# Performance work log

Hardware: AMD Instinct MI355X
Metric: run time of the kernel (lower is better)

## Reference

```python
import jax, jax.numpy as jnp
import numpy as np

CC_ITERS = 60  # min-label propagation + pointer doubling; covers huge diameters


def setup_inputs() -> dict:
    key = jax.random.key(0)
    k1, k2, k3, k4, k5 = jax.random.split(key, 5)
    N, C, E = 100000, 128, 800000
    x = jax.random.normal(k1, (N, C), jnp.float32)
    src = jax.random.randint(k2, (E,), 0, N)
    off = jax.random.randint(k3, (E,), 1, N)
    dst = (src + off) % N  # guarantees no self-loops (torch forward filters them)
    edge_index = jnp.stack([src, dst]).astype(jnp.int32)
    batch = jnp.zeros((N,), jnp.int32)
    W = jax.random.normal(k4, (2 * C,), jnp.float32) * 0.05
    b = (jax.random.normal(k5, (), jnp.float32) * 0.05).astype(jnp.float32)
    return {"x": x, "edge_index": edge_index, "batch": batch, "W": W, "b": b}


def _connected_components(src, dst, mask, N):
    # min-label propagation along selected edges, with path compression.
    def body(i, labels):
        ls = jnp.where(mask, labels[src], N)
        ld = jnp.where(mask, labels[dst], N)
        new = labels.at[dst].min(ls).at[src].min(ld)
        return jnp.minimum(new, new[new])  # pointer doubling
    return jax.lax.fori_loop(0, CC_ITERS, body, jnp.arange(N))


def reference(x, edge_index, batch, W, b):
    N, C = x.shape
    E = edge_index.shape[1]
    src, dst = edge_index[0], edge_index[1]

    # raw edge score: Linear(cat(x[src], x[dst])) without materializing the concat
    e = x[src] @ W[:C] + x[dst] @ W[C:] + b  # [E]
    # softmax over incoming edges of each dst node (segment softmax)
    m = jax.ops.segment_max(e, dst, num_segments=N)
    z = jnp.exp(e - m[dst])
    s = jax.ops.segment_sum(z, dst, num_segments=N)
    score = z / s[dst] + 0.5  # add_to_edge_score

    # edge selection (E > N -> quantile branch, matching torch)
    if E > N:
        q = 1.0 - (N // 2) / E
        mask = score > jnp.quantile(score, q)
    else:
        mask = score >= jnp.median(score)

    # weighted pairwise node reps for selected edges (masked instead of gathered)
    w = jnp.where(mask, score, 0.0)
    reps = (x[src] + x[dst]) * w[:, None]  # [E, C]
    mi = mask.astype(x.dtype)
    cnt = jnp.zeros((N,), x.dtype).at[src].add(mi).at[dst].add(mi)  # bincount of selected endpoints
    merged = cnt > 0
    base = jnp.where(merged[:, None], 0.0, x)  # merged nodes zeroed, untouched nodes keep x
    acc = base.at[src].add(reps).at[dst].add(reps)
    nodes = jnp.where(merged[:, None], acc / jnp.maximum(cnt, 1.0)[:, None], acc)

    # connected components over selected edges; relabel by first-occurrence order
    labels = _connected_components(src, dst, jax.lax.stop_gradient(mask), N)
    uniq = jnp.unique(labels, size=N, fill_value=N)
    cluster = jnp.searchsorted(uniq, labels)  # [N]

    new_x = jax.ops.segment_sum(nodes, cluster, num_segments=N)  # padded to N clusters

    # coalesce cluster-mapped edges: sorted unique pairs, padded with -1
    c0, c1 = cluster[src], cluster[dst]
    keys = jnp.unique(c0.astype(jnp.int64) * N + c1.astype(jnp.int64), size=E, fill_value=-1)
    valid = keys >= 0
    new_edge_index = jnp.stack([
        jnp.where(valid, keys // N, -1),
        jnp.where(valid, keys % N, -1),
    ])
    new_batch = jnp.zeros((N,), batch.dtype).at[cluster].set(batch)
    return new_x, new_edge_index, new_batch, score
```

## Files before the change

### kernel.cpp

```cpp
#include <hip/hip_runtime.h>
#include <math.h>
#include <stdint.h>

typedef unsigned long long u64;
typedef unsigned int u32;

#define NN 100000
#define CF 128
#define EE 800000

#define CAP 131072

#define EBITS 11
#define ERADIX 2048
#define STILE 2048
#define NB_E 391
#define SORT_N (NB_E * STILE)
#define MBITS 12
#define MRADIX 4096
#define NB_M 49
#define MSORT_N (NB_M * STILE)
#define HISTG_LEN 800768

#define SCTILE 2048
#define MCHUNK 16

#define ZSCALE 4503599627370496.0
#define XSCALE 32768.0f
#define XINV   (1.0f / 32768.0f)

struct Sel { u32 prefix; u32 k; };

__device__ inline u64 encD(double v) {
  u64 u = (u64)__double_as_longlong(v);
  return u ^ ((u >> 63) ? ~0ULL : 0x8000000000000000ULL);
}
__device__ inline double decD(u64 u) {
  u ^= ((u >> 63) ? 0x8000000000000000ULL : ~0ULL);
  return __longlong_as_double((long long)u);
}

__global__ void k_pq(const float* __restrict__ x, const float* __restrict__ W,
                     double* __restrict__ p, double* __restrict__ q) {
  int node = blockIdx.x * 4 + (threadIdx.x >> 6);
  int lane = threadIdx.x & 63;
  if (node >= NN) return;
  const float* xr = x + (size_t)node * CF;
  double a = (double)xr[lane] * (double)W[lane] + (double)xr[lane + 64] * (double)W[lane + 64];
  double c = (double)xr[lane] * (double)W[CF + lane] + (double)xr[lane + 64] * (double)W[CF + lane + 64];
  for (int off = 32; off; off >>= 1) { a += __shfl_xor(a, off); c += __shfl_xor(c, off); }
  if (lane == 0) { p[node] = a; q[node] = c; }
}

__global__ void k_em(const int* __restrict__ ei, const double* __restrict__ p,
                     const double* __restrict__ q, const float* __restrict__ bptr,
                     double* __restrict__ e, u64* __restrict__ menc) {
  int j = blockIdx.x * 256 + threadIdx.x;
  if (j >= EE) return;
  int s = ei[j], d = ei[EE + j];
  double ev = p[s] + q[d] + (double)bptr[0];
  e[j] = ev;
  atomicMax(&menc[d], encD(ev));
}

__global__ void k_zs(const int* __restrict__ ei, double* __restrict__ e,
                     const u64* __restrict__ menc, u64* __restrict__ sdenFx) {
  int j = blockIdx.x * 256 + threadIdx.x;
  if (j >= EE) return;
  int d = ei[EE + j];
  double z = exp(e[j] - decD(menc[d]));
  e[j] = z;
  atomicAdd(&sdenFx[d], (u64)__double2ll_rn(z * ZSCALE));
}

__global__ void k_score(const int* __restrict__ ei, const double* __restrict__ z,
                        const u64* __restrict__ sdenFx, float* __restrict__ outScore) {
  int j = blockIdx.x * 256 + threadIdx.x;
  if (j >= EE) return;
  int d = ei[EE + j];
  double s = (double)sdenFx[d] * (1.0 / ZSCALE);
  outScore[j] = (float)(z[j] / s + 0.5);
}

__global__ void k_selInit(Sel* st, u32* hist, int k0, int k1) {
  int t = blockIdx.x * 256 + threadIdx.x;
  if (t == 0) { st[0].prefix = 0x3Fu; st[0].k = (u32)k0; st[1].prefix = 0x3Fu; st[1].k = (u32)k1; }
  if (t < 512) hist[t] = 0;
}

__global__ void k_selHist(const float* __restrict__ score, const Sel* __restrict__ st,
                          u32* __restrict__ hist, int shift) {
  __shared__ u32 h[512];
  for (int i = threadIdx.x; i < 512; i += 256) h[i] = 0;
  __syncthreads();
  u32 p0 = st[0].prefix, p1 = st[1].prefix;
  for (int j = blockIdx.x * 256 + threadIdx.x; j < EE; j += gridDim.x * 256) {
    u32 u = __float_as_uint(score[j]);
    u32 d = (u >> shift) & 255u;
    if ((u >> (shift + 8)) == p0) atomicAdd(&h[d], 1u);
    if ((u >> (shift + 8)) == p1) atomicAdd(&h[256 + d], 1u);
  }
  __syncthreads();
  for (int i = threadIdx.x; i < 512; i += 256) if (h[i]) atomicAdd(&hist[i], h[i]);
}

__global__ void k_selPick(Sel* st, u32* hist) {
  if (threadIdx.x == 0) {
    for (int sel = 0; sel < 2; sel++) {
      u32 k = st[sel].k, cum = 0;
      for (int b = 0; b < 256; b++) {
        u32 c = hist[sel * 256 + b];
        if (cum + c > k) { st[sel].prefix = (st[sel].prefix << 8) | (u32)b; st[sel].k = k - cum; break; }
        cum += c;
      }
    }
  }
  __syncthreads();
  for (int i = threadIdx.x; i < 512; i += blockDim.x) hist[i] = 0;
}

__global__ void k_t(const Sel* st, float* tval, float frac) {
  float a = __uint_as_float(st[0].prefix);
  float b = __uint_as_float(st[1].prefix);
  tval[0] = __fadd_rn(a, __fmul_rn(__fsub_rn(b, a), frac));
}

__global__ void __launch_bounds__(1024) k_compact(
    const float* __restrict__ score, const float* __restrict__ tval,
    const int* __restrict__ ei, int* __restrict__ selCount,
    int* __restrict__ selSrc, int* __restrict__ selDst,
    float* __restrict__ selW, int* __restrict__ cnt) {
  __shared__ int wbase[16];
  int j = blockIdx.x * 1024 + threadIdx.x;
  int lane = threadIdx.x & 63;
  int wid = threadIdx.x >> 6;
  float sc = 0.0f;
  bool sel = false;
  if (j < EE) { sc = score[j]; sel = (sc > tval[0]); }
  u64 m = __ballot(sel);
  int wcnt = __popcll(m);
  int rank = __popcll(m & ((1ULL << lane) - 1ULL));
  if (lane == 0) wbase[wid] = wcnt;
  __syncthreads();
  if (threadIdx.x == 0) {
    int tot = 0;
#pragma unroll
    for (int w = 0; w < 16; w++) tot += wbase[w];
    int base = tot ? atomicAdd(selCount, tot) : 0;
#pragma unroll
    for (int w = 0; w < 16; w++) { int c = wbase[w]; wbase[w] = base; base += c; }
  }
  __syncthreads();
  if (sel) {
    int s = ei[j], d = ei[EE + j];
    int pos = wbase[wid] + rank;
    if (pos < CAP) { selSrc[pos] = s; selDst[pos] = d; selW[pos] = sc; }
    atomicAdd(&cnt[s], 1);
    atomicAdd(&cnt[d], 1);
  }
}

__global__ void k_labelInit(int* parent) {
  int i = blockIdx.x * 256 + threadIdx.x;
  if (i < NN) parent[i] = i;
}

__device__ inline int uf_find(int* parent, int x) {
  while (true) {
    int p = parent[x];
    if (p == x) return x;
    int gp = parent[p];
    if (gp == p) return p;
    parent[x] = gp;
    x = gp;
  }
}

__global__ void k_ufUnion(const int* __restrict__ selSrc, const int* __restrict__ selDst,
                          const int* __restrict__ selCount, int* __restrict__ parent) {
  int n = selCount[0]; if (n > CAP) n = CAP;
  for (int e = blockIdx.x * 256 + threadIdx.x; e < n; e += gridDim.x * 256) {
    int ru = uf_find(parent, selSrc[e]);
    int rv = uf_find(parent, selDst[e]);
    while (ru != rv) {
      if (ru < rv) { int t = ru; ru = rv; rv = t; }
      int old = atomicCAS(&parent[ru], ru, rv);
      if (old == ru) break;
      ru = uf_find(parent, old);
      rv = uf_find(parent, rv);
    }
  }
}

__global__ void k_ufFlattenRoots(int* __restrict__ parent, int* __restrict__ roots) {
  int i = blockIdx.x * 256 + threadIdx.x;
  if (i >= NN) return;
  int x = i;
  while (true) { int p = parent[x]; if (p == x) break; x = p; }
  parent[i] = x;
  roots[i] = (x == i) ? 1 : 0;
}

__global__ void k_clusterMkeys(const int* __restrict__ labels, const int* __restrict__ rootScan,
                               int* __restrict__ cluster, u64* __restrict__ mkeys) {
  int i = blockIdx.x * 256 + threadIdx.x;
  if (i < NN) {
    int cl = rootScan[labels[i]];
    cluster[i] = cl;
    mkeys[i] = ((u64)(u32)cl << 32) | (u32)i;
  } else if (i < MSORT_N) {
    mkeys[i] = ~0ULL;
  }
}

__global__ void k_scanBlock(const int* __restrict__ src, int* __restrict__ dst,
                            int n, int* __restrict__ bsums) {
  __shared__ int part[256];
  int base = blockIdx.x * SCTILE + threadIdx.x * 8;
  int v[8]; int s = 0;
#pragma unroll
  for (int i = 0; i < 8; i++) { v[i] = (base + i < n) ? src[base + i] : 0; s += v[i]; }
  part[threadIdx.x] = s;
  __syncthreads();
  for (int off = 1; off < 256; off <<= 1) {
    int t = (threadIdx.x >= off) ? part[threadIdx.x - off] : 0;
    __syncthreads();
    part[threadIdx.x] += t;
    __syncthreads();
  }
  int run = part[threadIdx.x] - s;
#pragma unroll
  for (int i = 0; i < 8; i++) { int vv = v[i]; if (base + i < n) dst[base + i] = run; run += vv; }
  if (threadIdx.x == 255) bsums[blockIdx.x] = part[255];
}
__global__ void k_scanTop(int* __restrict__ bsums, int nb) {
  __shared__ int part[256];
  int base = threadIdx.x * 4;
  int v[4]; int s = 0;
#pragma unroll
  for (int i = 0; i < 4; i++) { v[i] = (base + i < nb) ? bsums[base + i] : 0; s += v[i]; }
  part[threadIdx.x] = s;
  __syncthreads();
  for (int off = 1; off < 256; off <<= 1) {
    int t = (threadIdx.x >= off) ? part[threadIdx.x - off] : 0;
    __syncthreads();
    part[threadIdx.x] += t;
    __syncthreads();
  }
  int run = part[threadIdx.x] - s;
#pragma unroll
  for (int i = 0; i < 4; i++) { int vv = v[i]; if (base + i < nb) bsums[base + i] = run; run += vv; }
}
__global__ void k_scanAdd(int* __restrict__ data, int n, const int* __restrict__ bsums) {
  int add = bsums[blockIdx.x];
  int base = blockIdx.x * SCTILE + threadIdx.x * 8;
#pragma unroll
  for (int i = 0; i < 8; i++) if (base + i < n) data[base + i] += add;
}

template <typename K, int BITS>
__global__ void k_sortHistT(const K* __restrict__ keys, int* __restrict__ hist,
                            int shift, int nb) {
  const int RAD = 1 << BITS;
  __shared__ int h[RAD];
  for (int i = threadIdx.x; i < RAD; i += 256) h[i] = 0;
  __syncthreads();
  int base = blockIdx.x * STILE;
  for (int i = threadIdx.x; i < STILE; i += 256) {
    int d = (int)((keys[base + i] >> shift) & (RAD - 1));
    atomicAdd(&h[d], 1);
  }
  __syncthreads();
  for (int i = threadIdx.x; i < RAD; i += 256) hist[i * nb + blockIdx.x] = h[i];
}

template <typename K, int BITS>
__global__ void k_sortScatterT(const K* __restrict__ in, K* __restrict__ out,
                               const int* __restrict__ histScanned, int shift, int nb) {
  const int RAD = 1 << BITS;
  __shared__ int run[RAD];
  for (int i = threadIdx.x; i < RAD; i += 256) run[i] = 0;
  __syncthreads();
  int lane = threadIdx.x & 63;
  int wid = threadIdx.x >> 6;
  int base = blockIdx.x * STILE;
  for (int chunk = 0; chunk < 8; chunk++) {
    K key = in[base + chunk * 256 + threadIdx.x];
    int d = (int)((key >> shift) & (RAD - 1));
    u64 m = ~0ULL;
#pragma unroll
    for (int b = 0; b < BITS; b++) {
      u64 bal = __ballot((d >> b) & 1);
      m &= ((d >> b) & 1) ? bal : ~bal;
    }
    int laneRank = __popcll(m & ((1ULL << lane) - 1ULL));
    int cntm = __popcll(m);
    bool leader = (laneRank == 0);
    int local = 0;
    for (int w = 0; w < 4; w++) {
      if (wid == w) {
        int basev = run[d];
        local = basev + laneRank;
        if (leader) run[d] = basev + cntm;
      }
      __syncthreads();
    }
    out[histScanned[d * nb + blockIdx.x] + local] = key;
  }
}

__global__ void k_csr(const int* __restrict__ selSrc, const int* __restrict__ selDst,
                      const int* __restrict__ selCount, const int* __restrict__ nodeOff,
                      int* __restrict__ fill, int* __restrict__ edgeIdx) {
  int n = selCount[0]; if (n > CAP) n = CAP;
  for (int e = blockIdx.x * 256 + threadIdx.x; e < n; e += gridDim.x * 256) {
    int s = selSrc[e];
    int p = atomicAdd(&fill[s], 1);
    edgeIdx[nodeOff[s] + p] = e;
    int d = selDst[e];
    int p2 = atomicAdd(&fill[d], 1);
    edgeIdx[nodeOff[d] + p2] = e;
  }
}

__global__ void __launch_bounds__(128) k_clusterSum(
    const u64* __restrict__ mk, const int* __restrict__ nodeOff, const int* __restrict__ cnt,
    const int* __restrict__ edgeIdx, const int* __restrict__ selSrc,
    const int* __restrict__ selDst, const float* __restrict__ selW,
    const float* __restrict__ x, int* __restrict__ accX) {
  int c = threadIdx.x;
  int base = blockIdx.x * MCHUNK;
  if (base >= NN) return;
  int end = base + MCHUNK; if (end > NN) end = NN;
  u64 k0 = mk[base];
  int clN = (int)(k0 >> 32);
  int nodeN = (int)(k0 & 0xFFFFFFFFULL);
  int cntN = cnt[nodeN];
  int offN = nodeOff[nodeN];
  int curCl = -1; int acc = 0;
  for (int m = base; m < end; m++) {
    int cl = clN, ci = cntN, o = offN;
    if (m + 1 < end) {
      u64 k1 = mk[m + 1];
      clN = (int)(k1 >> 32);
      nodeN = (int)(k1 & 0xFFFFFFFFULL);
      cntN = cnt[nodeN];
      offN = nodeOff[nodeN];
    }
    if (ci == 0) continue;
    if (cl != curCl) {
      if (curCl >= 0 && acc != 0) atomicAdd(&accX[(size_t)curCl * CF + c], acc);
      curCl = cl; acc = 0;
    }
    int eN = edgeIdx[o];
    for (int t = 0; t < ci; t++) {
      int e = eN;
      if (t + 1 < ci) eN = edgeIdx[o + t + 1];
      float r = (x[(size_t)selSrc[e] * CF + c] + x[(size_t)selDst[e] * CF + c]) * selW[e];
      acc += __float2int_rn((r / (float)ci) * XSCALE);
    }
  }
  if (curCl >= 0 && acc != 0) atomicAdd(&accX[(size_t)curCl * CF + c], acc);
}

__global__ void k_final2(const int* __restrict__ accX, float* __restrict__ outNewX) {
  int t = (blockIdx.x * 256 + threadIdx.x) * 4;
  if (t >= NN * CF) return;
  int4 v = *(const int4*)(accX + t);
  float4 o;
  o.x = (float)v.x * XINV; o.y = (float)v.y * XINV;
  o.z = (float)v.z * XINV; o.w = (float)v.w * XINV;
  *(float4*)(outNewX + t) = o;
}

__global__ void k_copyUntouched(const float* __restrict__ x, const int* __restrict__ cnt,
                                const int* __restrict__ cluster, float* __restrict__ outNewX) {
  int t = blockIdx.x * 256 + threadIdx.x;
  if (t >= NN * CF) return;
  int i = t >> 7; int c = t & 127;
  if (cnt[i] == 0) outNewX[(size_t)cluster[i] * CF + c] = x[t];
}

__global__ void k_keysInit(const int* __restrict__ ei, const int* __restrict__ cluster,
                           u32* __restrict__ keys) {
  int t = blockIdx.x * 256 + threadIdx.x;
  if (t >= SORT_N) return;
  if (t < EE) {
    u32 kw = (u32)cluster[ei[t]] * 100000u + (u32)cluster[ei[EE + t]];
    keys[t] = kw ^ 0x80000000u;
  } else {
    keys[t] = 0xFFFFFFFFu;
  }
}

__global__ void k_flags(const u32* __restrict__ keys, int* __restrict__ f) {
  int j = blockIdx.x * 256 + threadIdx.x;
  if (j >= EE) return;
  f[j] = (j == 0 || keys[j] != keys[j - 1]) ? 1 : 0;
}
__global__ void k_eiFill(float* __restrict__ outEI) {
  int t = blockIdx.x * 256 + threadIdx.x;
  if (t < 2 * EE) outEI[t] = -1.0f;
}
__global__ void k_eiScatter(const u32* __restrict__ keys, const int* __restrict__ pos,
                            float* __restrict__ outEI) {
  int j = blockIdx.x * 256 + threadIdx.x;
  if (j >= EE) return;
  bool f = (j == 0 || keys[j] != keys[j - 1]);
  if (f) {
    int k32 = (int)(keys[j] ^ 0x80000000u);
    if (k32 >= 0) {
      int p = pos[j];
      outEI[p] = (float)(k32 / 100000);
      outEI[EE + p] = (float)(k32 % 100000);
    }
  }
}


static inline void runScan(int* data, int n, int* bsums, hipStream_t stream) {
  int nb = (n + SCTILE - 1) / SCTILE;
  k_scanBlock<<<nb, 256, 0, stream>>>(data, data, n, bsums);
  k_scanTop<<<1, 256, 0, stream>>>(bsums, nb);
  k_scanAdd<<<nb, 256, 0, stream>>>(data, n, bsums);
}
static inline void runScanFrom(const int* src, int* dst, int n, int* bsums, hipStream_t stream) {
  int nb = (n + SCTILE - 1) / SCTILE;
  k_scanBlock<<<nb, 256, 0, stream>>>(src, dst, n, bsums);
  k_scanTop<<<1, 256, 0, stream>>>(bsums, nb);
  k_scanAdd<<<nb, 256, 0, stream>>>(dst, n, bsums);
}

extern "C" void kernel_launch(void* const* d_in, const int* in_sizes, int n_in,
                              void* d_out, int out_size, void* d_ws, size_t ws_size,
                              hipStream_t stream) {
  const float* x = (const float*)d_in[0];
  const int* ei = (const int*)d_in[1];
  const float* W = (const float*)d_in[3];
  const float* bptr = (const float*)d_in[4];

  char* wp = (char*)d_ws;
  auto alloc = [&](size_t bytes) -> void* {
    void* r = (void*)wp;
    wp += (bytes + 255) & ~(size_t)255;
    return r;
  };
  double* ez = (double*)alloc((size_t)EE * 8);
  u32* sortA = (u32*)alloc((size_t)SORT_N * 4);
  u32* sortB = (u32*)alloc((size_t)SORT_N * 4);
  int* histG = (int*)alloc((size_t)HISTG_LEN * 4);
  int* fscan = (int*)alloc((size_t)EE * 4);
  double* p_d = (double*)alloc((size_t)NN * 8);
  double* q_d = (double*)alloc((size_t)NN * 8);
  u64* menc = (u64*)alloc((size_t)NN * 8);
  u64* sdenFx = (u64*)alloc((size_t)NN * 8);
  char* zeroAEnd = wp;
  int* accX = (int*)d_ws;
  const size_t ACCX_BYTES = (size_t)NN * CF * 4;
  if (wp < (char*)d_ws + ACCX_BYTES) wp = (char*)d_ws + ACCX_BYTES;
  int* cnt = (int*)alloc((size_t)NN * 4);
  int* fill = (int*)alloc((size_t)NN * 4);
  int* selCount = (int*)alloc(256);
  char* zeroBStart = (char*)cnt; char* zeroBEnd = wp;
  int* nodeOff = (int*)alloc((size_t)NN * 4);
  int* selSrc = (int*)alloc((size_t)CAP * 4);
  int* selDst = (int*)alloc((size_t)CAP * 4);
  float* selW = (float*)alloc((size_t)CAP * 4);
  int* labels = (int*)alloc((size_t)NN * 4);
  int* cluster = (int*)alloc((size_t)NN * 4);
  int* edgeIdx = (int*)alloc((size_t)CAP * 4);
  u64* mA = (u64*)alloc((size_t)MSORT_N * 8);
  u64* mB = (u64*)alloc((size_t)MSORT_N * 8);
  int* bsums = (int*)alloc(1024 * 4);
  Sel* st = (Sel*)alloc(256);
  u32* selHist = (u32*)alloc(512 * 4);
  float* tval = (float*)alloc(256);
  (void)ws_size; (void)n_in; (void)in_sizes;

  float* outNewX = (float*)d_out;
  float* outEI = outNewX + (size_t)NN * CF;
  float* outBatch = outEI + 2 * (size_t)EE;
  float* outScore = outBatch + NN;

  double qd = 1.0 - (double)(NN / 2) / (double)EE;
  double posd = qd * (double)(EE - 1);
  int k0 = (int)floor(posd);
  double fracd = posd - floor(posd);
  int k1 = (fracd > 0.0) ? k0 + 1 : k0;
  float frac = (float)fracd;

  hipMemsetAsync(outBatch, 0, (size_t)NN * 4, stream);
  hipMemsetAsync(menc, 0, (size_t)(zeroAEnd - (char*)menc), stream);
  hipMemsetAsync(zeroBStart, 0, (size_t)(zeroBEnd - zeroBStart), stream);

  k_pq<<<(NN + 3) / 4, 256, 0, stream>>>(x, W, p_d, q_d);
  k_em<<<(EE + 255) / 256, 256, 0, stream>>>(ei, p_d, q_d, bptr, ez, menc);
  k_zs<<<(EE + 255) / 256, 256, 0, stream>>>(ei, ez, menc, sdenFx);
  k_score<<<(EE + 255) / 256, 256, 0, stream>>>(ei, ez, sdenFx, outScore);

  k_selInit<<<2, 256, 0, stream>>>(st, selHist, k0, k1);
  for (int pass = 0; pass < 3; pass++) {
    k_selHist<<<1024, 256, 0, stream>>>(outScore, st, selHist, 16 - 8 * pass);
    k_selPick<<<1, 256, 0, stream>>>(st, selHist);
  }
  k_t<<<1, 64, 0, stream>>>(st, tval, frac);

  k_compact<<<(EE + 1023) / 1024, 1024, 0, stream>>>(outScore, tval, ei, selCount,
                                                     selSrc, selDst, selW, cnt);

  k_labelInit<<<(NN + 255) / 256, 256, 0, stream>>>(labels);
  k_ufUnion<<<256, 256, 0, stream>>>(selSrc, selDst, selCount, labels);
  k_ufUnion<<<256, 256, 0, stream>>>(selSrc, selDst, selCount, labels);
  k_ufFlattenRoots<<<(NN + 255) / 256, 256, 0, stream>>>(labels, fscan);

  runScan(fscan, NN, bsums, stream);
  k_clusterMkeys<<<(MSORT_N + 255) / 256, 256, 0, stream>>>(labels, fscan, cluster, mA);

  {
    u64* msin = mA; u64* msout = mB;
    for (int pass = 0; pass < 2; pass++) {
      int shift = 32 + MBITS * pass;
      k_sortHistT<u64, MBITS><<<NB_M, 256, 0, stream>>>(msin, histG, shift, NB_M);
      runScan(histG, MRADIX * NB_M, bsums, stream);
      k_sortScatterT<u64, MBITS><<<NB_M, 256, 0, stream>>>(msin, msout, histG, shift, NB_M);
      u64* tmp = msin; msin = msout; msout = tmp;
    }
  }
  u64* memberKeys = mA;

  k_keysInit<<<SORT_N / 256, 256, 0, stream>>>(ei, cluster, sortA);
  u32* sin = sortA; u32* sout = sortB;
  for (int pass = 0; pass < 3; pass++) {
    int shift = EBITS * pass;
    k_sortHistT<u32, EBITS><<<NB_E, 256, 0, stream>>>(sin, histG, shift, NB_E);
    runScan(histG, ERADIX * NB_E, bsums, stream);
    k_sortScatterT<u32, EBITS><<<NB_E, 256, 0, stream>>>(sin, sout, histG, shift, NB_E);
    u32* tmp = sin; sin = sout; sout = tmp;
  }
  k_flags<<<(EE + 255) / 256, 256, 0, stream>>>(sin, fscan);
  runScan(fscan, EE, bsums, stream);
  k_eiFill<<<(2 * EE + 255) / 256, 256, 0, stream>>>(outEI);
  k_eiScatter<<<(EE + 255) / 256, 256, 0, stream>>>(sin, fscan, outEI);

  runScanFrom(cnt, nodeOff, NN, bsums, stream);
  k_csr<<<256, 256, 0, stream>>>(selSrc, selDst, selCount, nodeOff, fill, edgeIdx);

  hipMemsetAsync(accX, 0, ACCX_BYTES, stream);
  k_clusterSum<<<(NN + MCHUNK - 1) / MCHUNK, 128, 0, stream>>>(
      memberKeys, nodeOff, cnt, edgeIdx, selSrc, selDst, selW, x, accX);
  k_final2<<<(NN * CF / 4 + 255) / 256, 256, 0, stream>>>(accX, outNewX);
  k_copyUntouched<<<(NN * CF + 255) / 256, 256, 0, stream>>>(x, cnt, cluster, outNewX);
}
```

Baseline: 703.0 us.

## Fuse small kernels, enlarge edge sort tiles, and merge final output passes

Several launches are folded into neighbouring kernels. The threshold computation moves into the last selection pick, label initialisation moves into compaction, and flag generation is fused into the scan's first stage. The untouched-node copy is merged into the final accumulator conversion via a per-cluster root-node map, and the edge radix sort now uses 4096-element tiles to halve block count and histogram size. The cluster-sum loop also software-pipelines the gather loads for the next edge. The aim is to cut launch overhead and extra passes over the N×C output, at the cost of an extra memset and per-element branching in the final kernel.

```diff
diff --git a/kernel.cpp b/kernel.cpp
--- a/kernel.cpp
+++ b/kernel.cpp
@@ -13,14 +13,15 @@
 
 #define EBITS 11
 #define ERADIX 2048
-#define STILE 2048
-#define NB_E 391
-#define SORT_N (NB_E * STILE)
+#define ETILE 4096
+#define NB_E 196
+#define SORT_N (NB_E * ETILE)
 #define MBITS 12
 #define MRADIX 4096
+#define MTILE 2048
 #define NB_M 49
-#define MSORT_N (NB_M * STILE)
-#define HISTG_LEN 800768
+#define MSORT_N (NB_M * MTILE)
+#define HISTG_LEN 401408
 
 #define SCTILE 2048
 #define MCHUNK 16
@@ -104,7 +105,7 @@
   for (int i = threadIdx.x; i < 512; i += 256) if (h[i]) atomicAdd(&hist[i], h[i]);
 }
 
-__global__ void k_selPick(Sel* st, u32* hist) {
+__global__ void k_selPick(Sel* st, u32* hist, float* tval, float frac, int last) {
   if (threadIdx.x == 0) {
     for (int sel = 0; sel < 2; sel++) {
       u32 k = st[sel].k, cum = 0;
@@ -114,24 +115,24 @@
         cum += c;
       }
     }
+    if (last) {
+      float a = __uint_as_float(st[0].prefix);
+      float b = __uint_as_float(st[1].prefix);
+      tval[0] = __fadd_rn(a, __fmul_rn(__fsub_rn(b, a), frac));
+    }
   }
   __syncthreads();
   for (int i = threadIdx.x; i < 512; i += blockDim.x) hist[i] = 0;
-}
-
-__global__ void k_t(const Sel* st, float* tval, float frac) {
-  float a = __uint_as_float(st[0].prefix);
-  float b = __uint_as_float(st[1].prefix);
-  tval[0] = __fadd_rn(a, __fmul_rn(__fsub_rn(b, a), frac));
 }
 
 __global__ void __launch_bounds__(1024) k_compact(
     const float* __restrict__ score, const float* __restrict__ tval,
     const int* __restrict__ ei, int* __restrict__ selCount,
     int* __restrict__ selSrc, int* __restrict__ selDst,
-    float* __restrict__ selW, int* __restrict__ cnt) {
+    float* __restrict__ selW, int* __restrict__ cnt, int* __restrict__ labels) {
   __shared__ int wbase[16];
   int j = blockIdx.x * 1024 + threadIdx.x;
+  if (j < NN) labels[j] = j;
   int lane = threadIdx.x & 63;
   int wid = threadIdx.x >> 6;
   float sc = 0.0f;
@@ -158,11 +159,6 @@
     atomicAdd(&cnt[s], 1);
     atomicAdd(&cnt[d], 1);
   }
-}
-
-__global__ void k_labelInit(int* parent) {
-  int i = blockIdx.x * 256 + threadIdx.x;
-  if (i < NN) parent[i] = i;
 }
 
 __device__ inline int uf_find(int* parent, int x) {
@@ -202,12 +198,14 @@
 }
 
 __global__ void k_clusterMkeys(const int* __restrict__ labels, const int* __restrict__ rootScan,
-                               int* __restrict__ cluster, u64* __restrict__ mkeys) {
+                               int* __restrict__ cluster, u64* __restrict__ mkeys,
+                               int* __restrict__ rootNode) {
   int i = blockIdx.x * 256 + threadIdx.x;
   if (i < NN) {
     int cl = rootScan[labels[i]];
     cluster[i] = cl;
     mkeys[i] = ((u64)(u32)cl << 32) | (u32)i;
+    if (labels[i] == i) rootNode[cl] = i;
   } else if (i < MSORT_N) {
     mkeys[i] = ~0ULL;
   }
@@ -233,12 +231,17 @@
   for (int i = 0; i < 8; i++) { int vv = v[i]; if (base + i < n) dst[base + i] = run; run += vv; }
   if (threadIdx.x == 255) bsums[blockIdx.x] = part[255];
 }
-__global__ void k_scanTop(int* __restrict__ bsums, int nb) {
+__global__ void k_scanFlags(const u32* __restrict__ keys, int* __restrict__ dst,
+                            int n, int* __restrict__ bsums) {
   __shared__ int part[256];
-  int base = threadIdx.x * 4;
-  int v[4]; int s = 0;
-#pragma unroll
-  for (int i = 0; i < 4; i++) { v[i] = (base + i < nb) ? bsums[base + i] : 0; s += v[i]; }
+  int base = blockIdx.x * SCTILE + threadIdx.x * 8;
+  int v[8]; int s = 0;
+#pragma unroll
+  for (int i = 0; i < 8; i++) {
+    int j = base + i;
+    v[i] = (j < n) ? ((j == 0 || keys[j] != keys[j - 1]) ? 1 : 0) : 0;
+    s += v[i];
+  }
   part[threadIdx.x] = s;
   __syncthreads();
   for (int off = 1; off < 256; off <<= 1) {
@@ -249,6 +252,25 @@
   }
   int run = part[threadIdx.x] - s;
 #pragma unroll
+  for (int i = 0; i < 8; i++) { int vv = v[i]; if (base + i < n) dst[base + i] = run; run += vv; }
+  if (threadIdx.x == 255) bsums[blockIdx.x] = part[255];
+}
+__global__ void k_scanTop(int* __restrict__ bsums, int nb) {
+  __shared__ int part[256];
+  int base = threadIdx.x * 4;
+  int v[4]; int s = 0;
+#pragma unroll
+  for (int i = 0; i < 4; i++) { v[i] = (base + i < nb) ? bsums[base + i] : 0; s += v[i]; }
+  part[threadIdx.x] = s;
+  __syncthreads();
+  for (int off = 1; off < 256; off <<= 1) {
+    int t = (threadIdx.x >= off) ? part[threadIdx.x - off] : 0;
+    __syncthreads();
+    part[threadIdx.x] += t;
+    __syncthreads();
+  }
+  int run = part[threadIdx.x] - s;
+#pragma unroll
   for (int i = 0; i < 4; i++) { int vv = v[i]; if (base + i < nb) bsums[base + i] = run; run += vv; }
 }
 __global__ void k_scanAdd(int* __restrict__ data, int n, const int* __restrict__ bsums) {
@@ -258,15 +280,15 @@
   for (int i = 0; i < 8; i++) if (base + i < n) data[base + i] += add;
 }
 
-template <typename K, int BITS>
+template <typename K, int BITS, int TILE>
 __global__ void k_sortHistT(const K* __restrict__ keys, int* __restrict__ hist,
                             int shift, int nb) {
   const int RAD = 1 << BITS;
   __shared__ int h[RAD];
   for (int i = threadIdx.x; i < RAD; i += 256) h[i] = 0;
   __syncthreads();
-  int base = blockIdx.x * STILE;
-  for (int i = threadIdx.x; i < STILE; i += 256) {
+  int base = blockIdx.x * TILE;
+  for (int i = threadIdx.x; i < TILE; i += 256) {
     int d = (int)((keys[base + i] >> shift) & (RAD - 1));
     atomicAdd(&h[d], 1);
   }
@@ -274,17 +296,18 @@
   for (int i = threadIdx.x; i < RAD; i += 256) hist[i * nb + blockIdx.x] = h[i];
 }
 
-template <typename K, int BITS>
+template <typename K, int BITS, int TILE>
 __global__ void k_sortScatterT(const K* __restrict__ in, K* __restrict__ out,
                                const int* __restrict__ histScanned, int shift, int nb) {
   const int RAD = 1 << BITS;
+  const int CH = TILE / 256;
   __shared__ int run[RAD];
   for (int i = threadIdx.x; i < RAD; i += 256) run[i] = 0;
   __syncthreads();
   int lane = threadIdx.x & 63;
   int wid = threadIdx.x >> 6;
-  int base = blockIdx.x * STILE;
-  for (int chunk = 0; chunk < 8; chunk++) {
+  int base = blockIdx.x * TILE;
+  for (int chunk = 0; chunk < CH; chunk++) {
     K key = in[base + chunk * 256 + threadIdx.x];
     int d = (int)((key >> shift) & (RAD - 1));
     u64 m = ~0ULL;
@@ -352,33 +375,43 @@
       if (curCl >= 0 && acc != 0) atomicAdd(&accX[(size_t)curCl * CF + c], acc);
       curCl = cl; acc = 0;
     }
-    int eN = edgeIdx[o];
+    int e0 = edgeIdx[o];
+    float w = selW[e0];
+    float xs = x[(size_t)selSrc[e0] * CF + c];
+    float xd = x[(size_t)selDst[e0] * CF + c];
     for (int t = 0; t < ci; t++) {
-      int e = eN;
-      if (t + 1 < ci) eN = edgeIdx[o + t + 1];
-      float r = (x[(size_t)selSrc[e] * CF + c] + x[(size_t)selDst[e] * CF + c]) * selW[e];
-      acc += __float2int_rn((r / (float)ci) * XSCALE);
+      float cur = (xs + xd) * w;
+      if (t + 1 < ci) {
+        int e1 = edgeIdx[o + t + 1];
+        w = selW[e1];
+        xs = x[(size_t)selSrc[e1] * CF + c];
+        xd = x[(size_t)selDst[e1] * CF + c];
+      }
+      acc += __float2int_rn((cur / (float)ci) * XSCALE);
     }
   }
   if (curCl >= 0 && acc != 0) atomicAdd(&accX[(size_t)curCl * CF + c], acc);
 }
 
-__global__ void k_final2(const int* __restrict__ accX, float* __restrict__ outNewX) {
+__global__ void k_finalFused(const float* __restrict__ x, const int* __restrict__ cnt,
+                             const int* __restrict__ rootNode, const int* __restrict__ accX,
+                             float* __restrict__ outNewX) {
   int t = (blockIdx.x * 256 + threadIdx.x) * 4;
   if (t >= NN * CF) return;
-  int4 v = *(const int4*)(accX + t);
+  int cl = t >> 7; int c = t & 127;
+  int r = rootNode[cl];
   float4 o;
-  o.x = (float)v.x * XINV; o.y = (float)v.y * XINV;
-  o.z = (float)v.z * XINV; o.w = (float)v.w * XINV;
+  if (r < 0) {
+    o.x = o.y = o.z = o.w = 0.0f;
+  } else if (cnt[r] == 0) {
+    const float* xr = x + (size_t)r * CF + c;
+    o.x = xr[0]; o.y = xr[1]; o.z = xr[2]; o.w = xr[3];
+  } else {
+    int4 v = *(const int4*)(accX + t);
+    o.x = (float)v.x * XINV; o.y = (float)v.y * XINV;
+    o.z = (float)v.z * XINV; o.w = (float)v.w * XINV;
+  }
   *(float4*)(outNewX + t) = o;
-}
-
-__global__ void k_copyUntouched(const float* __restrict__ x, const int* __restrict__ cnt,
-                                const int* __restrict__ cluster, float* __restrict__ outNewX) {
-  int t = blockIdx.x * 256 + threadIdx.x;
-  if (t >= NN * CF) return;
-  int i = t >> 7; int c = t & 127;
-  if (cnt[i] == 0) outNewX[(size_t)cluster[i] * CF + c] = x[t];
 }
 
 __global__ void k_keysInit(const int* __restrict__ ei, const int* __restrict__ cluster,
@@ -393,11 +426,6 @@
   }
 }
 
-__global__ void k_flags(const u32* __restrict__ keys, int* __restrict__ f) {
-  int j = blockIdx.x * 256 + threadIdx.x;
-  if (j >= EE) return;
-  f[j] = (j == 0 || keys[j] != keys[j - 1]) ? 1 : 0;
-}
 __global__ void k_eiFill(float* __restrict__ outEI) {
   int t = blockIdx.x * 256 + threadIdx.x;
   if (t < 2 * EE) outEI[t] = -1.0f;
@@ -462,6 +490,7 @@
   int* fill = (int*)alloc((size_t)NN * 4);
   int* selCount = (int*)alloc(256);
   char* zeroBStart = (char*)cnt; char* zeroBEnd = wp;
+  int* rootNode = (int*)alloc((size_t)NN * 4);
   int* nodeOff = (int*)alloc((size_t)NN * 4);
   int* selSrc = (int*)alloc((size_t)CAP * 4);
   int* selDst = (int*)alloc((size_t)CAP * 4);
@@ -492,6 +521,7 @@
   hipMemsetAsync(outBatch, 0, (size_t)NN * 4, stream);
   hipMemsetAsync(menc, 0, (size_t)(zeroAEnd - (char*)menc), stream);
   hipMemsetAsync(zeroBStart, 0, (size_t)(zeroBEnd - zeroBStart), stream);
+  hipMemsetAsync(rootNode, 0xFF, (size_t)NN * 4, stream);
 
   k_pq<<<(NN + 3) / 4, 256, 0, stream>>>(x, W, p_d, q_d);
   k_em<<<(EE + 255) / 256, 256, 0, stream>>>(ei, p_d, q_d, bptr, ez, menc);
@@ -501,28 +531,26 @@
   k_selInit<<<2, 256, 0, stream>>>(st, selHist, k0, k1);
   for (int pass = 0; pass < 3; pass++) {
     k_selHist<<<1024, 256, 0, stream>>>(outScore, st, selHist, 16 - 8 * pass);
-    k_selPick<<<1, 256, 0, stream>>>(st, selHist);
-  }
-  k_t<<<1, 64, 0, stream>>>(st, tval, frac);
+    k_selPick<<<1, 256, 0, stream>>>(st, selHist, tval, frac, pass == 2);
+  }
 
   k_compact<<<(EE + 1023) / 1024, 1024, 0, stream>>>(outScore, tval, ei, selCount,
-                                                     selSrc, selDst, selW, cnt);
-
-  k_labelInit<<<(NN + 255) / 256, 256, 0, stream>>>(labels);
+                                                     selSrc, selDst, selW, cnt, labels);
+
   k_ufUnion<<<256, 256, 0, stream>>>(selSrc, selDst, selCount, labels);
   k_ufUnion<<<256, 256, 0, stream>>>(selSrc, selDst, selCount, labels);
   k_ufFlattenRoots<<<(NN + 255) / 256, 256, 0, stream>>>(labels, fscan);
 
   runScan(fscan, NN, bsums, stream);
-  k_clusterMkeys<<<(MSORT_N + 255) / 256, 256, 0, stream>>>(labels, fscan, cluster, mA);
+  k_clusterMkeys<<<(MSORT_N + 255) / 256, 256, 0, stream>>>(labels, fscan, cluster, mA, rootNode);
 
   {
     u64* msin = mA; u64* msout = mB;
     for (int pass = 0; pass < 2; pass++) {
       int shift = 32 + MBITS * pass;
-      k_sortHistT<u64, MBITS><<<NB_M, 256, 0, stream>>>(msin, histG, shift, NB_M);
+      k_sortHistT<u64, MBITS, MTILE><<<NB_M, 256, 0, stream>>>(msin, histG, shift, NB_M);
       runScan(histG, MRADIX * NB_M, bsums, stream);
-      k_sortScatterT<u64, MBITS><<<NB_M, 256, 0, stream>>>(msin, msout, histG, shift, NB_M);
+      k_sortScatterT<u64, MBITS, MTILE><<<NB_M, 256, 0, stream>>>(msin, msout, histG, shift, NB_M);
       u64* tmp = msin; msin = msout; msout = tmp;
     }
   }
@@ -532,13 +560,17 @@
   u32* sin = sortA; u32* sout = sortB;
   for (int pass = 0; pass < 3; pass++) {
     int shift = EBITS * pass;
-    k_sortHistT<u32, EBITS><<<NB_E, 256, 0, stream>>>(sin, histG, shift, NB_E);
+    k_sortHistT<u32, EBITS, ETILE><<<NB_E, 256, 0, stream>>>(sin, histG, shift, NB_E);
     runScan(histG, ERADIX * NB_E, bsums, stream);
-    k_sortScatterT<u32, EBITS><<<NB_E, 256, 0, stream>>>(sin, sout, histG, shift, NB_E);
+    k_sortScatterT<u32, EBITS, ETILE><<<NB_E, 256, 0, stream>>>(sin, sout, histG, shift, NB_E);
     u32* tmp = sin; sin = sout; sout = tmp;
   }
-  k_flags<<<(EE + 255) / 256, 256, 0, stream>>>(sin, fscan);
-  runScan(fscan, EE, bsums, stream);
+  {
+    int nb = (EE + SCTILE - 1) / SCTILE;
+    k_scanFlags<<<nb, 256, 0, stream>>>(sin, fscan, EE, bsums);
+    k_scanTop<<<1, 256, 0, stream>>>(bsums, nb);
+    k_scanAdd<<<nb, 256, 0, stream>>>(fscan, EE, bsums);
+  }
   k_eiFill<<<(2 * EE + 255) / 256, 256, 0, stream>>>(outEI);
   k_eiScatter<<<(EE + 255) / 256, 256, 0, stream>>>(sin, fscan, outEI);
 
@@ -548,6 +580,5 @@
   hipMemsetAsync(accX, 0, ACCX_BYTES, stream);
   k_clusterSum<<<(NN + MCHUNK - 1) / MCHUNK, 128, 0, stream>>>(
       memberKeys, nodeOff, cnt, edgeIdx, selSrc, selDst, selW, x, accX);
-  k_final2<<<(NN * CF / 4 + 255) / 256, 256, 0, stream>>>(accX, outNewX);
-  k_copyUntouched<<<(NN * CF + 255) / 256, 256, 0, stream>>>(x, cnt, cluster, outNewX);
-}
+  k_finalFused<<<(NN * CF / 4 + 255) / 256, 256, 0, stream>>>(x, cnt, rootNode, accX, outNewX);
+}
```

New measurement: 686.1 us. 1.02x faster.
